# Optimization experiments

Measured on AMD Instinct MI355X. Metric: run time of the kernel, lower is better.

## Reference

```python
import jax, jax.numpy as jnp
import numpy as np

D = 512; E = 8; TOPK = 2; F = 2048; H = 4
SF_LEVELS = 4; SF_BASE = 4.0; LN_EPS = 1e-5


def _ln(h, s, b):
    mu = jnp.mean(h, axis=-1, keepdims=True)
    var = jnp.mean((h - mu) ** 2, axis=-1, keepdims=True)
    return (h - mu) / jnp.sqrt(var + LN_EPS) * s + b


def setup_inputs() -> dict:
    key = jax.random.key(0)
    ks = jax.random.split(key, 16)
    sc = 0.02
    inp = {
        "x": jax.random.normal(ks[0], (4, 1024, D), jnp.float32),
        "gate_w": jax.random.normal(ks[1], (D, E), jnp.float32) * sc,
        "gate_b": jnp.zeros((E,), jnp.float32),
        "ln1_s": jnp.ones((E, D), jnp.float32),
        "ln1_b": jnp.zeros((E, D), jnp.float32),
        "ln2_s": jnp.ones((E, D), jnp.float32),
        "ln2_b": jnp.zeros((E, D), jnp.float32),
        "wq": jax.random.normal(ks[2], (E, D, D), jnp.float32) * sc,
        "wk": jax.random.normal(ks[3], (E, D, D), jnp.float32) * sc,
        "wv": jax.random.normal(ks[4], (E, D, D), jnp.float32) * sc,
        "wo": jax.random.normal(ks[5], (E, D, D), jnp.float32) * sc,
        "bq": jnp.zeros((E, D), jnp.float32),
        "bk": jnp.zeros((E, D), jnp.float32),
        "bv": jnp.zeros((E, D), jnp.float32),
        "bo": jnp.zeros((E, D), jnp.float32),
        "w1": jax.random.normal(ks[6], (E, D, F), jnp.float32) * sc,
        "b1": jnp.zeros((E, F), jnp.float32),
        "w2": jax.random.normal(ks[7], (E, F, D), jnp.float32) * sc,
        "b2": jnp.zeros((E, D), jnp.float32),
    }
    return inp


def reference(x, gate_w, gate_b, ln1_s, ln1_b, ln2_s, ln2_b, wq, wk, wv, wo, bq, bk, bv, bo, w1, b1, w2, b2):
    B, S, d = x.shape
    dh = d // H
    # --- SpikingRouter ---
    logits = x @ gate_w + gate_b                       # [B,S,E]
    _, idx = jax.lax.top_k(logits, TOPK)               # [B,S,k]
    in_topk = jnp.sum(jax.nn.one_hot(idx, E, dtype=logits.dtype), axis=-2) > 0
    routing_in = jnp.where(in_topk, jax.nn.relu(logits), 0.0)
    # Scale-and-Fire neuron: multi-level threshold quantization
    mem = routing_in
    rw = jnp.zeros_like(mem)
    for lvl in range(SF_LEVELS):
        thr = SF_BASE / (2.0 ** lvl)
        spk = (mem >= thr).astype(mem.dtype)
        rw = rw + spk * thr
        mem = mem - spk * thr
    # --- all experts (SFormerBlock, post-norm transformer block) ---
    def block(p):
        l1s, l1b, l2s, l2b, Wq, Wk, Wv, Wo, Bq, Bk, Bv, Bo, W1, B1, W2, B2 = p
        q = (x @ Wq + Bq).reshape(B, S, H, dh)
        k = (x @ Wk + Bk).reshape(B, S, H, dh)
        v = (x @ Wv + Bv).reshape(B, S, H, dh)
        scores = jnp.einsum('bqhd,bkhd->bhqk', q, k) / jnp.sqrt(jnp.asarray(dh, x.dtype))
        att = jax.nn.softmax(scores, axis=-1)
        o = jnp.einsum('bhqk,bkhd->bqhd', att, v).reshape(B, S, d) @ Wo + Bo
        h = _ln(x + o, l1s, l1b)
        f = jax.nn.relu(h @ W1 + B1) @ W2 + B2
        return _ln(h + f, l2s, l2b)

    expert_outs = jax.vmap(block)((ln1_s, ln1_b, ln2_s, ln2_b, wq, wk, wv, wo, bq, bk, bv, bo, w1, b1, w2, b2))  # [E,B,S,D]
    final = jnp.einsum('ebsd,bse->bsd', expert_outs, rw)
    return final, logits
```

## Files before the change

### kernel.cpp

```cpp
#include <hip/hip_runtime.h>
#include <hip/hip_bf16.h>
#include <stdint.h>

using u16 = unsigned short;
typedef float floatx4 __attribute__((ext_vector_type(4)));
typedef __bf16 bfv8 __attribute__((ext_vector_type(8)));

#define AS1 __attribute__((address_space(1)))
#define AS3 __attribute__((address_space(3)))

__device__ __forceinline__ u16 f2bf_bits(float f) {
    __hip_bfloat16 h = __float2bfloat16(f);
    u16 u;
    __builtin_memcpy(&u, &h, 2);
    return u;
}
__device__ __forceinline__ float bf_bits2f(u16 u) {
    __hip_bfloat16 h;
    __builtin_memcpy(&h, &u, 2);
    return __bfloat162float(h);
}
__device__ __forceinline__ void gload_lds16(const void* g, void* l) {
    __builtin_amdgcn_global_load_lds((AS1 void*)(uintptr_t)g, (AS3 void*)l, 16, 0, 0);
}

__device__ __forceinline__ void stage64(const u16* __restrict__ Abase, long lda, const long* arow,
                                        const u16* __restrict__ Bb, long ldb, int k0, int tid,
                                        u16* Ad, u16* Bd) {
    #pragma unroll
    for (int j = 0; j < 4; ++j) {
        const int q   = j * 256 + tid;
        const int row = q >> 3;
        const int cg  = (q & 7) ^ (row & 7);
        gload_lds16(Abase + arow[j] * lda + k0 + cg * 8, Ad + q * 8);
        gload_lds16(Bb + (long)row * ldb + k0 + cg * 8, Bd + q * 8);
    }
}
__device__ __forceinline__ void compute64(const u16* Ab, const u16* Bb, int wy, int wx,
                                          int quad, int mrow, floatx4 acc[4][4]) {
    #pragma unroll
    for (int kk = 0; kk < 2; ++kk) {
        bfv8 af[4], bf[4];
        #pragma unroll
        for (int mi = 0; mi < 4; mi++) {
            const int r = wy * 64 + mi * 16 + mrow;
            const int slot = (kk * 4 + quad) ^ (r & 7);
            af[mi] = *(const bfv8*)&Ab[r * 64 + slot * 8];
        }
        #pragma unroll
        for (int ni = 0; ni < 4; ni++) {
            const int r = wx * 64 + ni * 16 + mrow;
            const int slot = (kk * 4 + quad) ^ (r & 7);
            bf[ni] = *(const bfv8*)&Bb[r * 64 + slot * 8];
        }
        #pragma unroll
        for (int mi = 0; mi < 4; mi++)
            #pragma unroll
            for (int ni = 0; ni < 4; ni++)
                acc[mi][ni] = __builtin_amdgcn_mfma_f32_16x16x32_bf16(af[mi], bf[ni], acc[mi][ni], 0, 0, 0);
    }
}

__global__ void cast_bf16_kernel(const float* __restrict__ in, u16* __restrict__ out, int n4,
                                 const float* __restrict__ bq, const float* __restrict__ bk,
                                 const float* __restrict__ bv, float* __restrict__ pb) {
    if (blockIdx.x >= 2048) {
        int j = (blockIdx.x - 2048) * 256 + threadIdx.x;
        const float* s = j < 4096 ? bq : (j < 8192 ? bk : bv);
        pb[j] = s[j & 4095];
        return;
    }
    int i = blockIdx.x * blockDim.x + threadIdx.x;
    if (i >= n4) return;
    float4 v = ((const float4*)in)[i];
    ushort4 o;
    o.x = f2bf_bits(v.x); o.y = f2bf_bits(v.y); o.z = f2bf_bits(v.z); o.w = f2bf_bits(v.w);
    ((ushort4*)out)[i] = o;
}

__global__ void transpose_cast_kernel(const float* __restrict__ src, u16* __restrict__ dst,
                                      int R, int C, long sSrc, long sDst) {
    __shared__ float tile[32][33];
    const float* s = src + (long)blockIdx.z * sSrc;
    u16* d = dst + (long)blockIdx.z * sDst;
    int c0 = blockIdx.x * 32, r0 = blockIdx.y * 32;
    int tx = threadIdx.x, ty = threadIdx.y;
    #pragma unroll
    for (int i = 0; i < 4; i++)
        tile[ty + 8*i][tx] = s[(long)(r0 + ty + 8*i) * C + c0 + tx];
    __syncthreads();
    #pragma unroll
    for (int i = 0; i < 4; i++)
        d[(long)(c0 + ty + 8*i) * R + r0 + tx] = f2bf_bits(tile[tx][ty + 8*i]);
}

__global__ void transpose_cast4_kernel(const float* __restrict__ w0, const float* __restrict__ w1p,
                                       const float* __restrict__ w2p, const float* __restrict__ w3p,
                                       u16* __restrict__ dst) {
    __shared__ float tile[32][33];
    int z = blockIdx.z;
    const float* s = (z < 8 ? w0 : z < 16 ? w1p : z < 24 ? w2p : w3p) + (long)(z & 7) * 262144;
    u16* d = dst + (long)z * 262144;
    int c0 = blockIdx.x * 32, r0 = blockIdx.y * 32;
    int tx = threadIdx.x, ty = threadIdx.y;
    #pragma unroll
    for (int i = 0; i < 4; i++)
        tile[ty + 8*i][tx] = s[(long)(r0 + ty + 8*i) * 512 + c0 + tx];
    __syncthreads();
    #pragma unroll
    for (int i = 0; i < 4; i++)
        d[(long)(c0 + ty + 8*i) * 512 + r0 + tx] = f2bf_bits(tile[tx][ty + 8*i]);
}

__global__ __launch_bounds__(512)
void router_kernel(const float* __restrict__ x, const float* __restrict__ gw,
                   const float* __restrict__ gb, float* __restrict__ rw,
                   float* __restrict__ logits_out) {
    int row = blockIdx.x;
    int w = threadIdx.x >> 6;
    int lane = threadIdx.x & 63;
    const float* xr = x + (long)row * 512;
    float sum = 0.f;
    #pragma unroll
    for (int i = 0; i < 8; i++) {
        int d = lane + 64 * i;
        sum += xr[d] * gw[d * 8 + w];
    }
    #pragma unroll
    for (int o = 32; o; o >>= 1) sum += __shfl_down(sum, o, 64);
    __shared__ float lg[8];
    if (lane == 0) lg[w] = sum + gb[w];
    __syncthreads();
    if (threadIdx.x == 0) {
        float l[8];
        #pragma unroll
        for (int e = 0; e < 8; e++) l[e] = lg[e];
        int i1 = 0;
        for (int e = 1; e < 8; e++) if (l[e] > l[i1]) i1 = e;
        int i2 = -1;
        for (int e = 0; e < 8; e++) { if (e == i1) continue; if (i2 < 0 || l[e] > l[i2]) i2 = e; }
        for (int e = 0; e < 8; e++) {
            float v = (e == i1 || e == i2) ? (l[e] > 0.f ? l[e] : 0.f) : 0.f;
            float r = 0.f, mem = v;
            #pragma unroll
            for (int lvl = 0; lvl < 4; lvl++) {
                float thr = 4.0f / (float)(1 << lvl);
                if (mem >= thr) { r += thr; mem -= thr; }
            }
            rw[(long)row * 8 + e] = r;
            logits_out[(long)row * 8 + e] = l[e];
        }
    }
}

__global__ __launch_bounds__(256)
void build_lists_kernel(const float* __restrict__ rw, int* __restrict__ prix,
                        int* __restrict__ act, int* __restrict__ smap,
                        int* __restrict__ tmap, int* __restrict__ tt, int* __restrict__ pt) {
    int b = blockIdx.x;
    int t = threadIdx.x, wv = t >> 6, lane = t & 63;
    __shared__ int wsum[4];
    __shared__ int base_sh;
    if (t == 0) base_sh = 0;
    __syncthreads();
    for (int e = 0; e < 8; e++) {
        int r0 = b * 1024 + t * 4;
        int f[4], c = 0;
        #pragma unroll
        for (int i = 0; i < 4; i++) {
            f[i] = (rw[(long)(r0 + i) * 8 + e] != 0.f) ? 1 : 0;
            c += f[i];
        }
        int incl = c;
        #pragma unroll
        for (int o = 1; o < 64; o <<= 1) {
            int n = __shfl_up(incl, o, 64);
            if (lane >= o) incl += n;
        }
        if (lane == 63) wsum[wv] = incl;
        __syncthreads();
        int woff = 0;
        #pragma unroll
        for (int k = 0; k < 4; k++) if (k < wv) woff += wsum[k];
        int tot = wsum[0] + wsum[1] + wsum[2] + wsum[3];
        int excl = incl - c + woff;
        int base = base_sh;
        int slot = excl;
        #pragma unroll
        for (int i = 0; i < 4; i++) {
            int r = r0 + i;
            if (f[i]) {
                int ps = base + slot;
                prix[b * 3072 + ps] = r;
                act[b * 3072 + ps] = 1;
                smap[(long)r * 8 + e] = ps;
                slot++;
            } else {
                smap[(long)r * 8 + e] = -1;
            }
        }
        int pad = (tot + 127) & ~127;
        for (int s = tot + t; s < pad; s += 256) {
            prix[b * 3072 + base + s] = b * 1024;
            act[b * 3072 + base + s] = 0;
        }
        for (int k = t; k < (pad >> 7); k += 256)
            tmap[b * 32 + (base >> 7) + k] = e;
        __syncthreads();
        if (t == 0) base_sh = base + pad;
        __syncthreads();
    }
    if (t == 0) {
        tt[b] = base_sh >> 7;
        pt[b] = base_sh;
    }
}

template<bool TRANSC>
__global__ __launch_bounds__(256)
void gemm_dense_kernel(const u16* __restrict__ A,
                       const u16* __restrict__ B, long sB,
                       u16* __restrict__ C, long sC,
                       const float* __restrict__ bias, int K) {
    __shared__ __align__(16) u16 As[2][128 * 64];
    __shared__ __align__(16) u16 Bs[2][128 * 64];
    const int z = blockIdx.z;
    const u16* Bb = B + (long)z * sB + (long)blockIdx.x * 128 * 512;

    const int tid = threadIdx.x;
    const int w = tid >> 6, lane = tid & 63;
    const int wy = w >> 1, wx = w & 1;
    const int quad = lane >> 4, mrow = lane & 15;

    long arow[4];
    #pragma unroll
    for (int j = 0; j < 4; ++j) arow[j] = (long)blockIdx.y * 128 + ((j * 256 + tid) >> 3);

    floatx4 acc[4][4];
    #pragma unroll
    for (int i = 0; i < 4; i++)
        #pragma unroll
        for (int j = 0; j < 4; j++)
            acc[i][j] = floatx4{0.f, 0.f, 0.f, 0.f};

    const int nk = K >> 6;
    stage64(A, 512, arow, Bb, 512, 0, tid, As[0], Bs[0]);
    for (int it = 0; it < nk; ++it) {
        const int cur = it & 1;
        __syncthreads();
        if (it + 1 < nk)
            stage64(A, 512, arow, Bb, 512, (it + 1) << 6, tid, As[1 - cur], Bs[1 - cur]);
        compute64(As[cur], Bs[cur], wy, wx, quad, mrow, acc);
    }

    const float* biasb = bias + (long)z * 512 + blockIdx.x * 128;
    if constexpr (TRANSC) {
        u16* Cb = C + (long)z * sC;
        #pragma unroll
        for (int ni = 0; ni < 4; ni++) {
            const int colt = wx * 64 + ni * 16 + mrow;
            const int n = blockIdx.x * 128 + colt;
            float bv = biasb[colt];
            #pragma unroll
            for (int mi = 0; mi < 4; mi++) {
                #pragma unroll
                for (int r = 0; r < 4; r++) {
                    const int m = blockIdx.y * 128 + wy * 64 + mi * 16 + quad * 4 + r;
                    float v = acc[mi][ni][r] + bv;
                    long addr = ((long)(((m >> 10) << 2) + (n >> 7)) * 128 + (n & 127)) * 1024 + (m & 1023);
                    Cb[addr] = f2bf_bits(v);
                }
            }
        }
    } else {
        u16* Cb = C + (long)z * sC + (long)blockIdx.y * 128 * 512 + blockIdx.x * 128;
        #pragma unroll
        for (int ni = 0; ni < 4; ni++) {
            const int col = wx * 64 + ni * 16 + mrow;
            float bv = biasb[col];
            #pragma unroll
            for (int mi = 0; mi < 4; mi++) {
                #pragma unroll
                for (int r = 0; r < 4; r++) {
                    const int row = wy * 64 + mi * 16 + quad * 4 + r;
                    Cb[(long)row * 512 + col] = f2bf_bits(acc[mi][ni][r] + bv);
                }
            }
        }
    }
}

__global__ __launch_bounds__(256)
void gemm_scores_kernel(const u16* __restrict__ QP, const u16* __restrict__ Km, u16* __restrict__ S,
                        const int* __restrict__ tmap, const int* __restrict__ tt,
                        float* __restrict__ psum, float alpha) {
    const int b = blockIdx.z >> 2, h = blockIdx.z & 3;
    const int tile = blockIdx.y;
    if (tile >= tt[b]) return;
    const int e = tmap[b * 32 + tile];
    __shared__ __align__(16) u16 As[2][128 * 64];
    __shared__ __align__(16) u16 Bs[2][128 * 64];
    __shared__ float psh[2][128];
    const u16* Abase = QP + (long)b * 3072 * 512 + h * 128;
    const u16* Bb = Km + ((long)e * 4096 + b * 1024 + blockIdx.x * 128) * 512 + h * 128;

    const int tid = threadIdx.x;
    const int w = tid >> 6, lane = tid & 63;
    const int wy = w >> 1, wx = w & 1;
    const int quad = lane >> 4, mrow = lane & 15;

    long arow[4];
    #pragma unroll
    for (int j = 0; j < 4; ++j)
        arow[j] = tile * 128 + ((j * 256 + tid) >> 3);

    floatx4 acc[4][4];
    #pragma unroll
    for (int i = 0; i < 4; i++)
        #pragma unroll
        for (int j = 0; j < 4; j++)
            acc[i][j] = floatx4{0.f, 0.f, 0.f, 0.f};

    stage64(Abase, 512, arow, Bb, 512, 0, tid, As[0], Bs[0]);
    for (int it = 0; it < 2; ++it) {
        const int cur = it & 1;
        __syncthreads();
        if (it == 0)
            stage64(Abase, 512, arow, Bb, 512, 64, tid, As[1], Bs[1]);
        compute64(As[cur], Bs[cur], wy, wx, quad, mrow, acc);
    }

    #pragma unroll
    for (int mi = 0; mi < 4; mi++) {
        #pragma unroll
        for (int r = 0; r < 4; r++) {
            float s = 0.f;
            #pragma unroll
            for (int ni = 0; ni < 4; ni++) {
                float p = __expf(acc[mi][ni][r] * alpha);
                acc[mi][ni][r] = p;
                s += p;
            }
            #pragma unroll
            for (int o = 1; o < 16; o <<= 1) s += __shfl_xor(s, o, 64);
            if (mrow == 0) psh[wx][wy * 64 + mi * 16 + quad * 4 + r] = s;
        }
    }
    __syncthreads();
    if (tid < 128) {
        long prow = (long)blockIdx.z * 3072 + tile * 128 + tid;
        psum[prow * 8 + blockIdx.x] = psh[0][tid] + psh[1][tid];
    }

    u16* Cb = S + ((long)blockIdx.z * 3072 + tile * 128) * 1024 + blockIdx.x * 128;
    #pragma unroll
    for (int ni = 0; ni < 4; ni++) {
        const int col = wx * 64 + ni * 16 + mrow;
        #pragma unroll
        for (int mi = 0; mi < 4; mi++) {
            #pragma unroll
            for (int r = 0; r < 4; r++) {
                const int row = wy * 64 + mi * 16 + quad * 4 + r;
                Cb[(long)row * 1024 + col] = f2bf_bits(acc[mi][ni][r]);
            }
        }
    }
}

__global__ __launch_bounds__(256)
void gemm_pv_kernel(const u16* __restrict__ S, const u16* __restrict__ VT, u16* __restrict__ OC,
                    const int* __restrict__ tmap, const int* __restrict__ tt,
                    const float* __restrict__ psum) {
    const int b = blockIdx.z >> 2, h = blockIdx.z & 3;
    const int tile = blockIdx.y;
    if (tile >= tt[b]) return;
    const int e = tmap[b * 32 + tile];
    __shared__ __align__(16) u16 As[2][128 * 64];
    __shared__ __align__(16) u16 Bs[2][128 * 64];
    __shared__ float invs[128];
    const u16* Abase = S + ((long)blockIdx.z * 3072 + tile * 128) * 1024;
    const u16* Bb = VT + ((long)e * 16 + blockIdx.z) * 131072;

    const int tid = threadIdx.x;
    const int w = tid >> 6, lane = tid & 63;
    const int wy = w >> 1, wx = w & 1;
    const int quad = lane >> 4, mrow = lane & 15;

    if (tid < 128) {
        const float* ps = psum + ((long)blockIdx.z * 3072 + tile * 128 + tid) * 8;
        float s = 0.f;
        #pragma unroll
        for (int i = 0; i < 8; i++) s += ps[i];
        invs[tid] = 1.f / s;
    }

    long arow[4];
    #pragma unroll
    for (int j = 0; j < 4; ++j) arow[j] = (j * 256 + tid) >> 3;

    floatx4 acc[4][4];
    #pragma unroll
    for (int i = 0; i < 4; i++)
        #pragma unroll
        for (int j = 0; j < 4; j++)
            acc[i][j] = floatx4{0.f, 0.f, 0.f, 0.f};

    stage64(Abase, 1024, arow, Bb, 1024, 0, tid, As[0], Bs[0]);
    for (int it = 0; it < 16; ++it) {
        const int cur = it & 1;
        __syncthreads();
        if (it + 1 < 16)
            stage64(Abase, 1024, arow, Bb, 1024, (it + 1) << 6, tid, As[1 - cur], Bs[1 - cur]);
        compute64(As[cur], Bs[cur], wy, wx, quad, mrow, acc);
    }

    u16* Cb = OC + ((long)b * 3072 + tile * 128) * 512 + h * 128;
    #pragma unroll
    for (int ni = 0; ni < 4; ni++) {
        const int col = wx * 64 + ni * 16 + mrow;
        #pragma unroll
        for (int mi = 0; mi < 4; mi++) {
            #pragma unroll
            for (int r = 0; r < 4; r++) {
                const int row = wy * 64 + mi * 16 + quad * 4 + r;
                Cb[(long)row * 512 + col] = f2bf_bits(acc[mi][ni][r] * invs[row]);
            }
        }
    }
}

template<bool RELU, bool GATHER>
__global__ __launch_bounds__(256)
void gemm_packed_kernel(const u16* __restrict__ A, int lda,
                        const u16* __restrict__ B, int ldb, long sBe,
                        u16* __restrict__ C, int ldc,
                        const float* __restrict__ bias, long sBiasE,
                        const int* __restrict__ tmap, const int* __restrict__ tt, int K,
                        const int* __restrict__ prix) {
    const int b = blockIdx.y / 24, tile = blockIdx.y % 24;
    if (tile >= tt[b]) return;
    const int e = tmap[b * 32 + tile];
    __shared__ __align__(16) u16 As[2][128 * 64];
    __shared__ __align__(16) u16 Bs[2][128 * 64];
    const long rbase = (long)b * 3072 + tile * 128;
    const u16* Ab = GATHER ? A : A + rbase * lda;
    const u16* Bb = B + (long)e * sBe + (long)blockIdx.x * 128 * ldb;

    const int tid = threadIdx.x;
    const int w = tid >> 6, lane = tid & 63;
    const int wy = w >> 1, wx = w & 1;
    const int quad = lane >> 4, mrow = lane & 15;

    long arow[4];
    #pragma unroll
    for (int j = 0; j < 4; ++j) {
        const int lr = (j * 256 + tid) >> 3;
        arow[j] = GATHER ? (long)prix[b * 3072 + tile * 128 + lr] : (long)lr;
    }

    floatx4 acc[4][4];
    #pragma unroll
    for (int i = 0; i < 4; i++)
        #pragma unroll
        for (int j = 0; j < 4; j++)
            acc[i][j] = floatx4{0.f, 0.f, 0.f, 0.f};

    const int nk = K >> 6;
    stage64(Ab, lda, arow, Bb, ldb, 0, tid, As[0], Bs[0]);
    for (int it = 0; it < nk; ++it) {
        const int cur = it & 1;
        __syncthreads();
        if (it + 1 < nk)
            stage64(Ab, lda, arow, Bb, ldb, (it + 1) << 6, tid, As[1 - cur], Bs[1 - cur]);
        compute64(As[cur], Bs[cur], wy, wx, quad, mrow, acc);
    }

    u16* Cb = C + rbase * ldc + (long)blockIdx.x * 128;
    const float* biasb = bias + (long)e * sBiasE + blockIdx.x * 128;
    #pragma unroll
    for (int ni = 0; ni < 4; ni++) {
        const int col = wx * 64 + ni * 16 + mrow;
        float bv = biasb[col];
        #pragma unroll
        for (int mi = 0; mi < 4; mi++) {
            #pragma unroll
            for (int r = 0; r < 4; r++) {
                const int row = wy * 64 + mi * 16 + quad * 4 + r;
                float v = acc[mi][ni][r] + bv;
                if (RELU) v = fmaxf(v, 0.f);
                Cb[(long)row * ldc + col] = f2bf_bits(v);
            }
        }
    }
}

__global__ __launch_bounds__(128)
void ln1_kernel(const float* __restrict__ x, const u16* __restrict__ tc,
                const int* __restrict__ prix, const int* __restrict__ act,
                const int* __restrict__ tmap, const int* __restrict__ pt,
                const float* __restrict__ s_all, const float* __restrict__ b_all,
                u16* __restrict__ hb) {
    int blk = blockIdx.x;
    int b = blk / 3072, pslot = blk % 3072;
    if (pslot >= pt[b]) return;
    long row = (long)b * 3072 + pslot;
    int tid = threadIdx.x, w = tid >> 6, lane = tid & 63;
    if (!act[row]) {
        *(ushort4*)(hb + row * 512 + tid * 4) = make_ushort4(0, 0, 0, 0);
        return;
    }
    int r = prix[row];
    int e = tmap[b * 32 + (pslot >> 7)];
    float4 xv = *(const float4*)(x + (long)r * 512 + tid * 4);
    ushort4 tu = *(const ushort4*)(tc + row * 512 + tid * 4);
    float v[4] = {xv.x + bf_bits2f(tu.x), xv.y + bf_bits2f(tu.y),
                  xv.z + bf_bits2f(tu.z), xv.w + bf_bits2f(tu.w)};
    float sum = v[0] + v[1] + v[2] + v[3];
    #pragma unroll
    for (int o = 32; o; o >>= 1) sum += __shfl_down(sum, o, 64);
    __shared__ float sh[4];
    if (lane == 0) sh[w] = sum;
    __syncthreads();
    float mu = (sh[0] + sh[1]) * (1.f / 512.f);
    float sq = 0.f;
    #pragma unroll
    for (int j = 0; j < 4; j++) { float d = v[j] - mu; sq += d * d; }
    #pragma unroll
    for (int o = 32; o; o >>= 1) sq += __shfl_down(sq, o, 64);
    if (lane == 0) sh[2 + w] = sq;
    __syncthreads();
    float inv = 1.f / sqrtf((sh[2] + sh[3]) * (1.f / 512.f) + 1e-5f);
    float4 sv = *(const float4*)(s_all + e * 512 + tid * 4);
    float4 bv = *(const float4*)(b_all + e * 512 + tid * 4);
    ushort4 ub;
    ub.x = f2bf_bits((v[0] - mu) * inv * sv.x + bv.x);
    ub.y = f2bf_bits((v[1] - mu) * inv * sv.y + bv.y);
    ub.z = f2bf_bits((v[2] - mu) * inv * sv.z + bv.z);
    ub.w = f2bf_bits((v[3] - mu) * inv * sv.w + bv.w);
    *(ushort4*)(hb + row * 512 + tid * 4) = ub;
}

__global__ __launch_bounds__(128)
void ln2acc_kernel(const u16* __restrict__ hb, const u16* __restrict__ t2,
                   const float* __restrict__ s_all, const float* __restrict__ b_all,
                   const float* __restrict__ rw, const int* __restrict__ smap,
                   float* __restrict__ out) {
    long r = blockIdx.x;
    int b = (int)(r >> 10);
    int tid = threadIdx.x, w = tid >> 6, lane = tid & 63;
    __shared__ float sh[4];
    float4 acc = make_float4(0.f, 0.f, 0.f, 0.f);
    for (int e = 0; e < 8; e++) {
        int ps = smap[r * 8 + e];
        if (ps >= 0) {
            float wgt = rw[r * 8 + e];
            long row = (long)b * 3072 + ps;
            ushort4 hu = *(const ushort4*)(hb + row * 512 + tid * 4);
            ushort4 fu = *(const ushort4*)(t2 + row * 512 + tid * 4);
            float v[4] = {bf_bits2f(hu.x) + bf_bits2f(fu.x), bf_bits2f(hu.y) + bf_bits2f(fu.y),
                          bf_bits2f(hu.z) + bf_bits2f(fu.z), bf_bits2f(hu.w) + bf_bits2f(fu.w)};
            float sum = v[0] + v[1] + v[2] + v[3];
            #pragma unroll
            for (int o = 32; o; o >>= 1) sum += __shfl_down(sum, o, 64);
            if (lane == 0) sh[w] = sum;
            __syncthreads();
            float mu = (sh[0] + sh[1]) * (1.f / 512.f);
            float sq = 0.f;
            #pragma unroll
            for (int j = 0; j < 4; j++) { float d = v[j] - mu; sq += d * d; }
            #pragma unroll
            for (int o = 32; o; o >>= 1) sq += __shfl_down(sq, o, 64);
            if (lane == 0) sh[2 + w] = sq;
            __syncthreads();
            float inv = 1.f / sqrtf((sh[2] + sh[3]) * (1.f / 512.f) + 1e-5f);
            float4 sv = *(const float4*)(s_all + e * 512 + tid * 4);
            float4 bv = *(const float4*)(b_all + e * 512 + tid * 4);
            acc.x += wgt * ((v[0] - mu) * inv * sv.x + bv.x);
            acc.y += wgt * ((v[1] - mu) * inv * sv.y + bv.y);
            acc.z += wgt * ((v[2] - mu) * inv * sv.z + bv.z);
            acc.w += wgt * ((v[3] - mu) * inv * sv.w + bv.w);
            __syncthreads();
        }
    }
    *(float4*)(out + r * 512 + tid * 4) = acc;
}

static const size_t WB_B   = 0;
static const size_t RW_B   = 50331648;
static const size_t PB_B   = 50462720;
static const size_t TT_B   = 50511872;
static const size_t PT_B   = 50511888;
static const size_t TMAP_B = 50511904;
static const size_t PRIX_B = 50512416;
static const size_t ACT_B  = 50561568;
static const size_t SMAP_B = 50610720;
static const size_t XB_B   = 50741792;
static const size_t Q8_B   = 54936096;
static const size_t K8_B   = 88490528;
static const size_t VT_B   = 122044960;
static const size_t S_B    = 155599392;
static const size_t PSUM_B = 256262688;
static const size_t OC_B   = Q8_B;
static const size_t TC_B   = K8_B;
static const size_t HB_B   = Q8_B;
static const size_t MID_B  = S_B;
static const size_t T2_B   = VT_B;

extern "C" void kernel_launch(void* const* d_in, const int* in_sizes, int n_in,
                              void* d_out, int out_size, void* d_ws, size_t ws_size,
                              hipStream_t stream) {
    const float* x      = (const float*)d_in[0];
    const float* gate_w = (const float*)d_in[1];
    const float* gate_b = (const float*)d_in[2];
    const float* ln1_s  = (const float*)d_in[3];
    const float* ln1_b  = (const float*)d_in[4];
    const float* ln2_s  = (const float*)d_in[5];
    const float* ln2_b  = (const float*)d_in[6];
    const float* wq = (const float*)d_in[7];
    const float* wk = (const float*)d_in[8];
    const float* wv = (const float*)d_in[9];
    const float* wo = (const float*)d_in[10];
    const float* bo = (const float*)d_in[14];
    const float* w1 = (const float*)d_in[15];
    const float* b1 = (const float*)d_in[16];
    const float* w2 = (const float*)d_in[17];
    const float* b2 = (const float*)d_in[18];
    float* out = (float*)d_out;

    char* ws = (char*)d_ws;
    u16*   WB   = (u16*)(ws + WB_B);
    float* RW   = (float*)(ws + RW_B);
    float* PB   = (float*)(ws + PB_B);
    int*   TT   = (int*)(ws + TT_B);
    int*   PT   = (int*)(ws + PT_B);
    int*   TMAP = (int*)(ws + TMAP_B);
    int*   PRIX = (int*)(ws + PRIX_B);
    int*   ACT  = (int*)(ws + ACT_B);
    int*   SMAP = (int*)(ws + SMAP_B);
    u16*   XB   = (u16*)(ws + XB_B);
    u16*   QP   = (u16*)(ws + Q8_B);
    u16*   K8   = (u16*)(ws + K8_B);
    u16*   VT8  = (u16*)(ws + VT_B);
    u16*   S    = (u16*)(ws + S_B);
    float* PSUM = (float*)(ws + PSUM_B);
    u16*   OC   = (u16*)(ws + OC_B);
    u16*   TC   = (u16*)(ws + TC_B);
    u16*   HB   = (u16*)(ws + HB_B);
    u16*   MID  = (u16*)(ws + MID_B);
    u16*   T2   = (u16*)(ws + T2_B);

    cast_bf16_kernel<<<dim3(2096), 256, 0, stream>>>(x, XB, 4096 * 512 / 4,
                                                     (const float*)d_in[11], (const float*)d_in[12],
                                                     (const float*)d_in[13], PB);
    transpose_cast4_kernel<<<dim3(16,16,32), dim3(32,8), 0, stream>>>(wq, wk, wv, wo, WB);
    transpose_cast_kernel<<<dim3(64,16,8), dim3(32,8), 0, stream>>>(w1, WB + 8388608,  512,  2048, 1048576, 1048576);
    transpose_cast_kernel<<<dim3(16,64,8), dim3(32,8), 0, stream>>>(w2, WB + 16777216, 2048, 512,  1048576, 1048576);
    router_kernel<<<4096, 512, 0, stream>>>(x, gate_w, gate_b, RW, out + 2097152);
    build_lists_kernel<<<4, 256, 0, stream>>>(RW, PRIX, ACT, SMAP, TMAP, TT, PT);

    const float isq = 0.08838834764831845f;

    gemm_dense_kernel<false><<<dim3(4,32,8), 256, 0, stream>>>(
        XB, WB + 2097152, 262144, K8, 2097152, PB + 4096, 512);
    gemm_dense_kernel<true><<<dim3(4,32,8), 256, 0, stream>>>(
        XB, WB + 4194304, 262144, VT8, 2097152, PB + 8192, 512);
    gemm_packed_kernel<false, true><<<dim3(4,96), 256, 0, stream>>>(
        XB, 512, WB, 512, 262144, QP, 512, PB, 512, TMAP, TT, 512, PRIX);

    gemm_scores_kernel<<<dim3(8,24,16), 256, 0, stream>>>(
        QP, K8, S, TMAP, TT, PSUM, isq);
    gemm_pv_kernel<<<dim3(1,24,16), 256, 0, stream>>>(S, VT8, OC, TMAP, TT, PSUM);

    gemm_packed_kernel<false, false><<<dim3(4,96), 256, 0, stream>>>(
        OC, 512, WB + 6291456, 512, 262144, TC, 512, bo, 512, TMAP, TT, 512, nullptr);
    ln1_kernel<<<12288, 128, 0, stream>>>(x, TC, PRIX, ACT, TMAP, PT, ln1_s, ln1_b, HB);
    gemm_packed_kernel<true, false><<<dim3(16,96), 256, 0, stream>>>(
        HB, 512, WB + 8388608, 512, 1048576, MID, 2048, b1, 2048, TMAP, TT, 512, nullptr);
    gemm_packed_kernel<false, false><<<dim3(4,96), 256, 0, stream>>>(
        MID, 2048, WB + 16777216, 2048, 1048576, T2, 512, b2, 512, TMAP, TT, 2048, nullptr);
    ln2acc_kernel<<<4096, 128, 0, stream>>>(HB, T2, ln2_s, ln2_b, RW, SMAP, out);
}
```

Before: 477.0 us.

## Fuse attention scores and PV into a single flash-style kernel

Replaces the separate scores kernel, which wrote bf16 probabilities to global memory, and the PV kernel with one fused kernel. Q fragments stay in registers, K and V tiles are streamed through LDS, exp(P) is written to LDS and multiplied by V, and row sums are accumulated in registers. This removes the large S and PSUM round-trip through global memory and one launch. In exchange it has less grid parallelism (384 blocks instead of 3072+384), adds more syncthreads per tile, and does no max-subtraction, which mirrors the before code.

```diff
diff --git a/kernel.cpp b/kernel.cpp
--- a/kernel.cpp
+++ b/kernel.cpp
@@ -36,6 +36,15 @@
         gload_lds16(Bb + (long)row * ldb + k0 + cg * 8, Bd + q * 8);
     }
 }
+__device__ __forceinline__ void stage_one(const u16* __restrict__ base, long ld, int tid, u16* dst) {
+    #pragma unroll
+    for (int j = 0; j < 4; ++j) {
+        const int q   = j * 256 + tid;
+        const int row = q >> 3;
+        const int cg  = (q & 7) ^ (row & 7);
+        gload_lds16(base + (long)row * ld + cg * 8, dst + q * 8);
+    }
+}
 __device__ __forceinline__ void compute64(const u16* Ab, const u16* Bb, int wy, int wx,
                                           int quad, int mrow, floatx4 acc[4][4]) {
     #pragma unroll
@@ -58,6 +67,24 @@
             #pragma unroll
             for (int ni = 0; ni < 4; ni++)
                 acc[mi][ni] = __builtin_amdgcn_mfma_f32_16x16x32_bf16(af[mi], bf[ni], acc[mi][ni], 0, 0, 0);
+    }
+}
+__device__ __forceinline__ void computeQK(const u16* Kb, const bfv8 qf[2][4], int wy,
+                                          int quad, int mrow, floatx4 acc[4][4]) {
+    #pragma unroll
+    for (int kk = 0; kk < 2; ++kk) {
+        bfv8 af[4];
+        #pragma unroll
+        for (int mi = 0; mi < 4; mi++) {
+            const int r = wy * 64 + mi * 16 + mrow;
+            const int slot = (kk * 4 + quad) ^ (r & 7);
+            af[mi] = *(const bfv8*)&Kb[r * 64 + slot * 8];
+        }
+        #pragma unroll
+        for (int mi = 0; mi < 4; mi++)
+            #pragma unroll
+            for (int ni = 0; ni < 4; ni++)
+                acc[mi][ni] = __builtin_amdgcn_mfma_f32_16x16x32_bf16(af[mi], qf[kk][ni], acc[mi][ni], 0, 0, 0);
     }
 }
 
@@ -290,141 +317,123 @@
     }
 }
 
-__global__ __launch_bounds__(256)
-void gemm_scores_kernel(const u16* __restrict__ QP, const u16* __restrict__ Km, u16* __restrict__ S,
-                        const int* __restrict__ tmap, const int* __restrict__ tt,
-                        float* __restrict__ psum, float alpha) {
-    const int b = blockIdx.z >> 2, h = blockIdx.z & 3;
-    const int tile = blockIdx.y;
+__global__ __launch_bounds__(256, 2)
+void attn_fused_kernel(const u16* __restrict__ QP, const u16* __restrict__ Km,
+                       const u16* __restrict__ VT, u16* __restrict__ OC,
+                       const int* __restrict__ tmap, const int* __restrict__ tt, float alpha) {
+    const int tile = blockIdx.x;
+    const int bh = blockIdx.y;
+    const int b = bh >> 2, h = bh & 3;
     if (tile >= tt[b]) return;
     const int e = tmap[b * 32 + tile];
-    __shared__ __align__(16) u16 As[2][128 * 64];
+
     __shared__ __align__(16) u16 Bs[2][128 * 64];
-    __shared__ float psh[2][128];
-    const u16* Abase = QP + (long)b * 3072 * 512 + h * 128;
-    const u16* Bb = Km + ((long)e * 4096 + b * 1024 + blockIdx.x * 128) * 512 + h * 128;
+    __shared__ __align__(16) u16 Ps[2][128 * 64];
+    __shared__ float rs_sh[2][128];
 
     const int tid = threadIdx.x;
     const int w = tid >> 6, lane = tid & 63;
     const int wy = w >> 1, wx = w & 1;
     const int quad = lane >> 4, mrow = lane & 15;
 
-    long arow[4];
-    #pragma unroll
-    for (int j = 0; j < 4; ++j)
-        arow[j] = tile * 128 + ((j * 256 + tid) >> 3);
-
-    floatx4 acc[4][4];
-    #pragma unroll
-    for (int i = 0; i < 4; i++)
-        #pragma unroll
-        for (int j = 0; j < 4; j++)
-            acc[i][j] = floatx4{0.f, 0.f, 0.f, 0.f};
-
-    stage64(Abase, 512, arow, Bb, 512, 0, tid, As[0], Bs[0]);
-    for (int it = 0; it < 2; ++it) {
-        const int cur = it & 1;
-        __syncthreads();
-        if (it == 0)
-            stage64(Abase, 512, arow, Bb, 512, 64, tid, As[1], Bs[1]);
-        compute64(As[cur], Bs[cur], wy, wx, quad, mrow, acc);
-    }
-
-    #pragma unroll
-    for (int mi = 0; mi < 4; mi++) {
-        #pragma unroll
-        for (int r = 0; r < 4; r++) {
-            float s = 0.f;
+    const u16* Qbase = QP + ((long)b * 3072 + tile * 128) * 512 + h * 128;
+    const u16* Kbase = Km + ((long)e * 4096 + b * 1024) * 512 + h * 128;
+    const u16* Vbase = VT + ((long)e * 16 + bh) * 131072;
+
+    stage_one(Qbase, 512, tid, Ps[0]);
+    stage_one(Qbase + 64, 512, tid, Ps[1]);
+    __syncthreads();
+    bfv8 qf[2][2][4];
+    #pragma unroll
+    for (int c = 0; c < 2; c++)
+        #pragma unroll
+        for (int kk = 0; kk < 2; kk++)
             #pragma unroll
             for (int ni = 0; ni < 4; ni++) {
-                float p = __expf(acc[mi][ni][r] * alpha);
-                acc[mi][ni][r] = p;
-                s += p;
+                const int r = wx * 64 + ni * 16 + mrow;
+                const int slot = (kk * 4 + quad) ^ (r & 7);
+                qf[c][kk][ni] = *(const bfv8*)&Ps[c][r * 64 + slot * 8];
             }
-            #pragma unroll
-            for (int o = 1; o < 16; o <<= 1) s += __shfl_xor(s, o, 64);
-            if (mrow == 0) psh[wx][wy * 64 + mi * 16 + quad * 4 + r] = s;
-        }
-    }
-    __syncthreads();
-    if (tid < 128) {
-        long prow = (long)blockIdx.z * 3072 + tile * 128 + tid;
-        psum[prow * 8 + blockIdx.x] = psh[0][tid] + psh[1][tid];
-    }
-
-    u16* Cb = S + ((long)blockIdx.z * 3072 + tile * 128) * 1024 + blockIdx.x * 128;
+
+    floatx4 acc_o[4][4];
+    float rsum[4];
+    #pragma unroll
+    for (int i = 0; i < 4; i++) {
+        rsum[i] = 0.f;
+        #pragma unroll
+        for (int j = 0; j < 4; j++) acc_o[i][j] = floatx4{0.f, 0.f, 0.f, 0.f};
+    }
+
+    for (int kt = 0; kt < 8; ++kt) {
+        __syncthreads();
+        stage_one(Kbase + (long)kt * 128 * 512,      512, tid, Bs[0]);
+        stage_one(Kbase + (long)kt * 128 * 512 + 64, 512, tid, Bs[1]);
+        __syncthreads();
+
+        floatx4 acc_s[4][4];
+        #pragma unroll
+        for (int i = 0; i < 4; i++)
+            #pragma unroll
+            for (int j = 0; j < 4; j++) acc_s[i][j] = floatx4{0.f, 0.f, 0.f, 0.f};
+        computeQK(Bs[0], qf[0], wy, quad, mrow, acc_s);
+        computeQK(Bs[1], qf[1], wy, quad, mrow, acc_s);
+
+        #pragma unroll
+        for (int mi = 0; mi < 4; mi++)
+            #pragma unroll
+            for (int ni = 0; ni < 4; ni++)
+                #pragma unroll
+                for (int r = 0; r < 4; r++) {
+                    float p = __expf(acc_s[mi][ni][r] * alpha);
+                    acc_s[mi][ni][r] = p;
+                    rsum[ni] += p;
+                }
+
+        __syncthreads();
+        stage_one(Vbase + kt * 128,      1024, tid, Bs[0]);
+        stage_one(Vbase + kt * 128 + 64, 1024, tid, Bs[1]);
+        u16* Pw = Ps[wy];
+        #pragma unroll
+        for (int mi = 0; mi < 4; mi++) {
+            const int sb = mi * 2 + (quad >> 1);
+            #pragma unroll
+            for (int ni = 0; ni < 4; ni++) {
+                const int q = wx * 64 + ni * 16 + mrow;
+                u16* pr = Pw + q * 64 + (sb ^ (q & 7)) * 8 + (quad & 1) * 4;
+                #pragma unroll
+                for (int r = 0; r < 4; r += 2) {
+                    uint32_t pk = (uint32_t)f2bf_bits(acc_s[mi][ni][r]) |
+                                  ((uint32_t)f2bf_bits(acc_s[mi][ni][r + 1]) << 16);
+                    *(uint32_t*)(pr + r) = pk;
+                }
+            }
+        }
+        __syncthreads();
+        compute64(Bs[0], Ps[0], wy, wx, quad, mrow, acc_o);
+        compute64(Bs[1], Ps[1], wy, wx, quad, mrow, acc_o);
+    }
+
     #pragma unroll
     for (int ni = 0; ni < 4; ni++) {
-        const int col = wx * 64 + ni * 16 + mrow;
+        float v = rsum[ni];
+        v += __shfl_xor(v, 16, 64);
+        v += __shfl_xor(v, 32, 64);
+        if (quad == 0) rs_sh[wy][wx * 64 + ni * 16 + mrow] = v;
+    }
+    __syncthreads();
+    u16* Cb = OC + ((long)b * 3072 + tile * 128) * 512 + h * 128;
+    #pragma unroll
+    for (int ni = 0; ni < 4; ni++) {
+        const int q = wx * 64 + ni * 16 + mrow;
+        const float inv = 1.f / (rs_sh[0][q] + rs_sh[1][q]);
         #pragma unroll
         for (int mi = 0; mi < 4; mi++) {
-            #pragma unroll
-            for (int r = 0; r < 4; r++) {
-                const int row = wy * 64 + mi * 16 + quad * 4 + r;
-                Cb[(long)row * 1024 + col] = f2bf_bits(acc[mi][ni][r]);
-            }
-        }
-    }
-}
-
-__global__ __launch_bounds__(256)
-void gemm_pv_kernel(const u16* __restrict__ S, const u16* __restrict__ VT, u16* __restrict__ OC,
-                    const int* __restrict__ tmap, const int* __restrict__ tt,
-                    const float* __restrict__ psum) {
-    const int b = blockIdx.z >> 2, h = blockIdx.z & 3;
-    const int tile = blockIdx.y;
-    if (tile >= tt[b]) return;
-    const int e = tmap[b * 32 + tile];
-    __shared__ __align__(16) u16 As[2][128 * 64];
-    __shared__ __align__(16) u16 Bs[2][128 * 64];
-    __shared__ float invs[128];
-    const u16* Abase = S + ((long)blockIdx.z * 3072 + tile * 128) * 1024;
-    const u16* Bb = VT + ((long)e * 16 + blockIdx.z) * 131072;
-
-    const int tid = threadIdx.x;
-    const int w = tid >> 6, lane = tid & 63;
-    const int wy = w >> 1, wx = w & 1;
-    const int quad = lane >> 4, mrow = lane & 15;
-
-    if (tid < 128) {
-        const float* ps = psum + ((long)blockIdx.z * 3072 + tile * 128 + tid) * 8;
-        float s = 0.f;
-        #pragma unroll
-        for (int i = 0; i < 8; i++) s += ps[i];
-        invs[tid] = 1.f / s;
-    }
-
-    long arow[4];
-    #pragma unroll
-    for (int j = 0; j < 4; ++j) arow[j] = (j * 256 + tid) >> 3;
-
-    floatx4 acc[4][4];
-    #pragma unroll
-    for (int i = 0; i < 4; i++)
-        #pragma unroll
-        for (int j = 0; j < 4; j++)
-            acc[i][j] = floatx4{0.f, 0.f, 0.f, 0.f};
-
-    stage64(Abase, 1024, arow, Bb, 1024, 0, tid, As[0], Bs[0]);
-    for (int it = 0; it < 16; ++it) {
-        const int cur = it & 1;
-        __syncthreads();
-        if (it + 1 < 16)
-            stage64(Abase, 1024, arow, Bb, 1024, (it + 1) << 6, tid, As[1 - cur], Bs[1 - cur]);
-        compute64(As[cur], Bs[cur], wy, wx, quad, mrow, acc);
-    }
-
-    u16* Cb = OC + ((long)b * 3072 + tile * 128) * 512 + h * 128;
-    #pragma unroll
-    for (int ni = 0; ni < 4; ni++) {
-        const int col = wx * 64 + ni * 16 + mrow;
-        #pragma unroll
-        for (int mi = 0; mi < 4; mi++) {
-            #pragma unroll
-            for (int r = 0; r < 4; r++) {
-                const int row = wy * 64 + mi * 16 + quad * 4 + r;
-                Cb[(long)row * 512 + col] = f2bf_bits(acc[mi][ni][r] * invs[row]);
-            }
+            ushort4 st;
+            st.x = f2bf_bits(acc_o[mi][ni][0] * inv);
+            st.y = f2bf_bits(acc_o[mi][ni][1] * inv);
+            st.z = f2bf_bits(acc_o[mi][ni][2] * inv);
+            st.w = f2bf_bits(acc_o[mi][ni][3] * inv);
+            *(ushort4*)(Cb + (long)q * 512 + wy * 64 + mi * 16 + quad * 4) = st;
         }
     }
 }
@@ -599,7 +608,6 @@
 static const size_t K8_B   = 88490528;
 static const size_t VT_B   = 122044960;
 static const size_t S_B    = 155599392;
-static const size_t PSUM_B = 256262688;
 static const size_t OC_B   = Q8_B;
 static const size_t TC_B   = K8_B;
 static const size_t HB_B   = Q8_B;
@@ -641,8 +649,6 @@
     u16*   QP   = (u16*)(ws + Q8_B);
     u16*   K8   = (u16*)(ws + K8_B);
     u16*   VT8  = (u16*)(ws + VT_B);
-    u16*   S    = (u16*)(ws + S_B);
-    float* PSUM = (float*)(ws + PSUM_B);
     u16*   OC   = (u16*)(ws + OC_B);
     u16*   TC   = (u16*)(ws + TC_B);
     u16*   HB   = (u16*)(ws + HB_B);
@@ -667,9 +673,7 @@
     gemm_packed_kernel<false, true><<<dim3(4,96), 256, 0, stream>>>(
         XB, 512, WB, 512, 262144, QP, 512, PB, 512, TMAP, TT, 512, PRIX);
 
-    gemm_scores_kernel<<<dim3(8,24,16), 256, 0, stream>>>(
-        QP, K8, S, TMAP, TT, PSUM, isq);
-    gemm_pv_kernel<<<dim3(1,24,16), 256, 0, stream>>>(S, VT8, OC, TMAP, TT, PSUM);
+    attn_fused_kernel<<<dim3(24, 16), 256, 0, stream>>>(QP, K8, VT8, OC, TMAP, TT, isq);
 
     gemm_packed_kernel<false, false><<<dim3(4,96), 256, 0, stream>>>(
         OC, 512, WB + 6291456, 512, 262144, TC, 512, bo, 512, TMAP, TT, 512, nullptr);
```

After: 440.8 us. 1.08x faster.
